# Kernel optimization log

Hardware: AMD Instinct MI355X
Metric: run time of the kernel (lower is better)

## Reference

```python
import jax, jax.numpy as jnp
import numpy as np

N_HEADS = 12

def setup_inputs() -> dict:
    key = jax.random.key(0)
    k1, k2, k3 = jax.random.split(key, 3)
    B, N, D = 2, 2048, 768
    x = jax.random.normal(k1, (B, N, D), dtype=jnp.float32)
    # Linear weights stored as [in, out] (equivalent to torch W.T)
    Wkqv = jax.random.normal(k2, (D, 3 * D), dtype=jnp.float32) * (1.0 / np.sqrt(D))
    bkqv = jnp.zeros((3 * D,), dtype=jnp.float32)
    Wproj = jax.random.normal(k3, (D, D), dtype=jnp.float32) * (1.0 / np.sqrt(D))
    bproj = jnp.zeros((D,), dtype=jnp.float32)
    return {"x": x, "Wkqv": Wkqv, "bkqv": bkqv, "Wproj": Wproj, "bproj": bproj}


def reference(x, Wkqv, bkqv, Wproj, bproj):
    B, N, D = x.shape
    H = N_HEADS
    hd = D // H
    kqv = x @ Wkqv + bkqv                     # [B, N, 3D]
    # NOTE: original chunks in (k, q, v) order
    k, q, v = jnp.split(kqv, 3, axis=-1)
    k = k.reshape(B, N, H, hd).transpose(0, 2, 1, 3)   # [B, H, N, hd]
    q = q.reshape(B, N, H, hd).transpose(0, 2, 1, 3)
    v = v.reshape(B, N, H, hd).transpose(0, 2, 1, 3)
    att = jnp.einsum('bhqd,bhkd->bhqk', q, k) / jnp.sqrt(jnp.float32(hd))
    causal = jnp.tril(jnp.ones((N, N), dtype=bool))    # [N, N]
    att = jnp.where(causal[None, None, :, :], att, jnp.float32(-jnp.inf))
    w = jax.nn.softmax(att, axis=-1)
    sa = jnp.einsum('bhqk,bhkd->bhqd', w, v)           # [B, H, N, hd]
    sa = sa.transpose(0, 2, 1, 3).reshape(B, N, D)
    return sa @ Wproj + bproj
```

## Files before the change

kernel.cpp:

```cpp
#include <hip/hip_runtime.h>

typedef __attribute__((ext_vector_type(8))) short bf16x8;
typedef __attribute__((ext_vector_type(16))) float f32x16;

#define BATCH 2
#define SEQ 2048
#define DMODEL 768
#define NH 12
#define HD 64
#define M_TOK (BATCH * SEQ)
#define N_KQV (3 * DMODEL)

#define GLOAD16(gsrc, ldst) __builtin_amdgcn_global_load_lds( \
    (const __attribute__((address_space(1))) unsigned int*)(const void*)(gsrc), \
    (__attribute__((address_space(3))) unsigned int*)(void*)(ldst), 16, 0, 0)

__device__ __forceinline__ unsigned short f2bf(float f) {
  unsigned int u = __float_as_uint(f);
  u += 0x7FFFu + ((u >> 16) & 1u);
  return (unsigned short)(u >> 16);
}

__device__ __forceinline__ unsigned int cvtpk(float lo, float hi) {
  unsigned int r;
  asm("v_cvt_pk_bf16_f32 %0, %1, %2" : "=v"(r) : "v"(lo), "v"(hi));
  return r;
}

#define NB_CVT 3072
#define NB_T1 (72 * 24)
#define NB_T2 (24 * 24)

__global__ __launch_bounds__(256) void prep_kernel(
    const float* __restrict__ x, unsigned short* __restrict__ x_bf,
    const float* __restrict__ Wkqv, unsigned short* __restrict__ wkqvT,
    const float* __restrict__ Wproj, unsigned short* __restrict__ wprojT) {
  const int b = blockIdx.x;
  if (b < NB_CVT) {
    int i = b * 256 + threadIdx.x;
    float4 v = reinterpret_cast<const float4*>(x)[i];
    unsigned long long p = (unsigned long long)f2bf(v.x)
                         | ((unsigned long long)f2bf(v.y) << 16)
                         | ((unsigned long long)f2bf(v.z) << 32)
                         | ((unsigned long long)f2bf(v.w) << 48);
    reinterpret_cast<unsigned long long*>(x_bf)[i] = p;
    return;
  }
  __shared__ float tile[32][33];
  const float* in;
  unsigned short* out;
  int rows, cols, bx, by;
  if (b < NB_CVT + NB_T1) {
    int j = b - NB_CVT;
    in = Wkqv; out = wkqvT; rows = DMODEL; cols = N_KQV;
    bx = j % 72; by = j / 72;
  } else {
    int j = b - NB_CVT - NB_T1;
    in = Wproj; out = wprojT; rows = DMODEL; cols = DMODEL;
    bx = j % 24; by = j / 24;
  }
  const int tx = threadIdx.x & 31, ty = threadIdx.x >> 5;
  int c0 = bx * 32, r0 = by * 32;
  for (int i = ty; i < 32; i += 8)
    tile[i][tx] = in[(size_t)(r0 + i) * cols + c0 + tx];
  __syncthreads();
  for (int i = ty; i < 32; i += 8)
    out[(size_t)(c0 + i) * rows + r0 + tx] = f2bf(tile[tx][i]);
}

template <int NBX, int MODE>
__global__ __launch_bounds__(64) void gemm_wi(
    const unsigned short* __restrict__ A,
    const unsigned short* __restrict__ BT,
    const float* __restrict__ bias,
    int NTOT,
    unsigned short* __restrict__ outK, unsigned short* __restrict__ outQ,
    unsigned short* __restrict__ outVT, float* __restrict__ outF) {
  constexpr int K = DMODEL;
  __shared__ __align__(16) unsigned short lds_a[2][64][32];
  __shared__ __align__(16) unsigned short lds_b[2][64][32];
  const int lane = threadIdx.x & 63;
  const int l31 = lane & 31, hi = lane >> 5;

  const int fid = (int)blockIdx.x;
  const int xcd = fid & 7, slot = fid >> 3;
  const int by = xcd * 8 + (slot & 7);
  const int bx = slot >> 3;
  const int m0 = by * 64, n0 = bx * 64;

  f32x16 acc[2][2];
#pragma unroll
  for (int mi = 0; mi < 2; mi++)
#pragma unroll
    for (int nj = 0; nj < 2; nj++)
#pragma unroll
      for (int i = 0; i < 16; i++) acc[mi][nj][i] = 0.f;

  const int srow = lane >> 2;
  const int sg = ((lane & 3) ^ ((lane >> 3) & 3)) * 8;
  const int xq = (l31 >> 1) & 3;

#define STAGE(buf, k0)                                                        \
  {                                                                           \
    _Pragma("unroll")                                                         \
    for (int rr = 0; rr < 4; ++rr)                                            \
      GLOAD16(&A[(size_t)(m0 + rr * 16 + srow) * K + (k0) + sg],              \
              &lds_a[buf][rr * 16][0]);                                       \
    _Pragma("unroll")                                                         \
    for (int rr = 0; rr < 4; ++rr)                                            \
      GLOAD16(&BT[(size_t)(n0 + rr * 16 + srow) * K + (k0) + sg],             \
              &lds_b[buf][rr * 16][0]);                                       \
  }

  const int KT = K >> 5;
  STAGE(0, 0);
  STAGE(1, 32);

  for (int kt = 0; kt < KT; ++kt) {
    const int cur = kt & 1;
    if (kt + 1 < KT) asm volatile("s_waitcnt vmcnt(8)" ::: "memory");
    else             asm volatile("s_waitcnt vmcnt(0)" ::: "memory");
    __builtin_amdgcn_sched_barrier(0);

    bf16x8 aA[2][2], aB[2][2];
#pragma unroll
    for (int ds = 0; ds < 2; ds++) {
      const int rc = ((ds * 2 + hi) ^ xq) * 8;
#pragma unroll
      for (int mi = 0; mi < 2; mi++)
        aA[ds][mi] = *(const bf16x8*)&lds_a[cur][mi * 32 + l31][rc];
#pragma unroll
      for (int nj = 0; nj < 2; nj++)
        aB[ds][nj] = *(const bf16x8*)&lds_b[cur][nj * 32 + l31][rc];
    }
#pragma unroll
    for (int ds = 0; ds < 2; ds++)
#pragma unroll
      for (int mi = 0; mi < 2; mi++)
#pragma unroll
        for (int nj = 0; nj < 2; nj++)
          acc[mi][nj] = __builtin_amdgcn_mfma_f32_32x32x16_bf16(
              aA[ds][mi], aB[ds][nj], acc[mi][nj], 0, 0, 0);

    if (kt + 2 < KT) {
      asm volatile("s_waitcnt lgkmcnt(0)" ::: "memory");
      __builtin_amdgcn_sched_barrier(0);
      STAGE(cur, (kt + 2) << 5);
    }
  }
#undef STAGE

#pragma unroll
  for (int mi = 0; mi < 2; mi++) {
#pragma unroll
    for (int nj = 0; nj < 2; nj++) {
#pragma unroll
      for (int r = 0; r < 16; r++) {
        int row = m0 + mi * 32 + (r & 3) + 8 * (r >> 2) + 4 * hi;
        int col = n0 + nj * 32 + l31;
        float v = acc[mi][nj][r] + bias[col];
        if (MODE == 0) {
          int chunk = col / DMODEL;
          int d = col - chunk * DMODEL;
          int hh = d >> 6, di = d & 63;
          int bb = row >> 11, tok = row & 2047;
          int bh = bb * NH + hh;
          if (chunk == 0)
            outK[((size_t)bh * SEQ + tok) * HD + di] = f2bf(v);
          else if (chunk == 1)
            outQ[((size_t)bh * SEQ + tok) * HD + di] = f2bf(v * 0.125f);
          else
            outVT[((size_t)bh * HD + di) * SEQ + tok] = f2bf(v);
        } else {
          outF[(size_t)row * NTOT + col] = v;
        }
      }
    }
  }
}

__global__ __launch_bounds__(128) void attn_kernel(
    const unsigned short* __restrict__ qbuf,
    const unsigned short* __restrict__ kbuf,
    const unsigned short* __restrict__ vT,
    unsigned short* __restrict__ sa) {
  __shared__ __align__(16) char smem_raw[18432];
  auto k_lds = reinterpret_cast<unsigned short (*)[72]>(smem_raw);
  auto v_lds = reinterpret_cast<unsigned short (*)[72]>(smem_raw + 9216);
  auto o_merge = reinterpret_cast<float (*)[32][33]>(smem_raw);
  auto l_merge = reinterpret_cast<float (*)[32]>(smem_raw + 9216);

  const int tid = threadIdx.x, lane = tid & 63, w = tid >> 6;
  const int l31 = lane & 31, hi = lane >> 5;

  const int fid = (int)blockIdx.y * (int)gridDim.x + (int)blockIdx.x;
  const int xcd = fid & 7, slot = fid >> 3;
  const int head3 = slot % 3;
  const int t = 63 - slot / 3;
  const int bh = head3 * 8 + xcd;
  const int ktmax = t >> 1;

  const size_t qk_base = (size_t)bh * SEQ * HD;
  const size_t v_base = (size_t)bh * HD * SEQ;
  const int bb = bh / NH, h = bh - bb * NH;

  const int sr = w * 32 + (lane >> 3);
  const int sc = (lane & 7) * 8;

  {
    bf16x8 rk[4], rv[4];
#pragma unroll
    for (int p = 0; p < 4; p++) {
      rk[p] = *(const bf16x8*)&kbuf[qk_base + (size_t)(sr + 8 * p) * HD + sc];
      rv[p] = *(const bf16x8*)&vT[v_base + (size_t)(sr + 8 * p) * SEQ + sc];
    }
#pragma unroll
    for (int p = 0; p < 4; p++) {
      *(bf16x8*)&k_lds[sr + 8 * p][sc] = rk[p];
      *(bf16x8*)&v_lds[sr + 8 * p][sc] = rv[p];
    }
  }

  bf16x8 aq[4];
#pragma unroll
  for (int ds = 0; ds < 4; ds++)
    aq[ds] = *(const bf16x8*)&qbuf[qk_base + (size_t)(t * 32 + l31) * HD + ds * 16 + hi * 8];

  f32x16 o0, o1;
#pragma unroll
  for (int i = 0; i < 16; i++) { o0[i] = 0.f; o1[i] = 0.f; }
  float lsum = 0.f;

  __syncthreads();

  for (int kt = 0; kt <= ktmax; ++kt) {
    const bool more = (kt < ktmax);
    bf16x8 rk[4], rv[4];
    if (more) {
      const int nrow = (kt + 1) * 64;
#pragma unroll
      for (int p = 0; p < 4; p++) {
        rk[p] = *(const bf16x8*)&kbuf[qk_base + (size_t)(nrow + sr + 8 * p) * HD + sc];
        rv[p] = *(const bf16x8*)&vT[v_base + (size_t)(sr + 8 * p) * SEQ + nrow + sc];
      }
    }

    f32x16 s;
#pragma unroll
    for (int i = 0; i < 16; i++) s[i] = 0.f;
    __builtin_amdgcn_s_setprio(1);
#pragma unroll
    for (int ds = 0; ds < 4; ds++) {
      bf16x8 bk = *(const bf16x8*)&k_lds[w * 32 + l31][ds * 16 + hi * 8];
      s = __builtin_amdgcn_mfma_f32_32x32x16_bf16(bk, aq[ds], s, 0, 0, 0);
    }
    __builtin_amdgcn_s_setprio(0);

    const bool diag = (kt == ktmax);
    const int qb2 = (t & 1) * 32;
#pragma unroll
    for (int r = 0; r < 16; r++) {
      int kr = (r & 3) + 8 * (r >> 2) + 4 * hi;
      float val = s[r];
      if (diag && (w * 32 + kr > qb2 + l31)) val = -1e30f;
      float p = __expf(val);
      s[r] = p;
      lsum += p;
    }

    union { unsigned int u[4]; bf16x8 v; } f1, f2;
    {
      unsigned int A = cvtpk(s[0], s[1]), B = cvtpk(s[2], s[3]);
      unsigned int C = cvtpk(s[4], s[5]), D = cvtpk(s[6], s[7]);
      auto rAC = __builtin_amdgcn_permlane32_swap(A, C, false, false);
      auto rBD = __builtin_amdgcn_permlane32_swap(B, D, false, false);
      f1.u[0] = rAC[0]; f1.u[1] = rBD[0]; f1.u[2] = rAC[1]; f1.u[3] = rBD[1];
      unsigned int A2 = cvtpk(s[8], s[9]),   B2 = cvtpk(s[10], s[11]);
      unsigned int C2 = cvtpk(s[12], s[13]), D2 = cvtpk(s[14], s[15]);
      auto rAC2 = __builtin_amdgcn_permlane32_swap(A2, C2, false, false);
      auto rBD2 = __builtin_amdgcn_permlane32_swap(B2, D2, false, false);
      f2.u[0] = rAC2[0]; f2.u[1] = rBD2[0]; f2.u[2] = rAC2[1]; f2.u[3] = rBD2[1];
    }

    __builtin_amdgcn_s_setprio(1);
    {
      bf16x8 bv00 = *(const bf16x8*)&v_lds[l31][w * 32 + hi * 8];
      bf16x8 bv01 = *(const bf16x8*)&v_lds[32 + l31][w * 32 + hi * 8];
      o0 = __builtin_amdgcn_mfma_f32_32x32x16_bf16(f1.v, bv00, o0, 0, 0, 0);
      o1 = __builtin_amdgcn_mfma_f32_32x32x16_bf16(f1.v, bv01, o1, 0, 0, 0);
      bf16x8 bv10 = *(const bf16x8*)&v_lds[l31][w * 32 + 16 + hi * 8];
      bf16x8 bv11 = *(const bf16x8*)&v_lds[32 + l31][w * 32 + 16 + hi * 8];
      o0 = __builtin_amdgcn_mfma_f32_32x32x16_bf16(f2.v, bv10, o0, 0, 0, 0);
      o1 = __builtin_amdgcn_mfma_f32_32x32x16_bf16(f2.v, bv11, o1, 0, 0, 0);
    }
    __builtin_amdgcn_s_setprio(0);

    if (more) {
      __syncthreads();
#pragma unroll
      for (int p = 0; p < 4; p++) {
        *(bf16x8*)&k_lds[sr + 8 * p][sc] = rk[p];
        *(bf16x8*)&v_lds[sr + 8 * p][sc] = rv[p];
      }
      __syncthreads();
    }
  }

  __syncthreads();
  {
    float ltot = lsum + __shfl_xor(lsum, 32);
    if (hi == 0) l_merge[w][l31] = ltot;
    f32x16 osend = w ? o0 : o1;
#pragma unroll
    for (int r = 0; r < 16; r++) {
      int ql = (r & 3) + 8 * (r >> 2) + 4 * hi;
      o_merge[w][ql][l31] = osend[r];
    }
    __syncthreads();
    f32x16 okeep = w ? o1 : o0;
#pragma unroll
    for (int r = 0; r < 16; r++) {
      int ql = (r & 3) + 8 * (r >> 2) + 4 * hi;
      float ot = okeep[r] + o_merge[1 - w][ql][l31];
      float lt = l_merge[0][ql] + l_merge[1][ql];
      sa[((size_t)bb * SEQ + t * 32 + ql) * DMODEL + h * HD + w * 32 + l31] = f2bf(ot / lt);
    }
  }
}


extern "C" void kernel_launch(void* const* d_in, const int* in_sizes, int n_in,
                              void* d_out, int out_size, void* d_ws, size_t ws_size,
                              hipStream_t stream) {
  const float* x     = (const float*)d_in[0];
  const float* Wkqv  = (const float*)d_in[1];
  const float* bkqv  = (const float*)d_in[2];
  const float* Wproj = (const float*)d_in[3];
  const float* bproj = (const float*)d_in[4];
  float* out = (float*)d_out;

  char* ws = (char*)d_ws;
  unsigned short* x_bf   = (unsigned short*)(ws + 0);
  unsigned short* wkqvT  = (unsigned short*)(ws + 6291456);
  unsigned short* wprojT = (unsigned short*)(ws + 9830400);
  unsigned short* qb     = (unsigned short*)(ws + 11010048);
  unsigned short* kb     = (unsigned short*)(ws + 17301504);
  unsigned short* vT     = (unsigned short*)(ws + 23592960);
  unsigned short* sa     = (unsigned short*)(ws + 29884416);

  prep_kernel<<<NB_CVT + NB_T1 + NB_T2, 256, 0, stream>>>(
      x, x_bf, Wkqv, wkqvT, Wproj, wprojT);

  gemm_wi<N_KQV / 64, 0><<<2304, 64, 0, stream>>>(
      x_bf, wkqvT, bkqv, N_KQV, kb, qb, vT, nullptr);

  attn_kernel<<<dim3(64, BATCH * NH), 128, 0, stream>>>(qb, kb, vT, sa);

  gemm_wi<DMODEL / 64, 1><<<768, 64, 0, stream>>>(
      sa, wprojT, bproj, DMODEL, nullptr, nullptr, nullptr, out);
}
```

Before: 99.73 us.

## Split attention over key chunks with atomic accumulation and a finalize pass

The attention kernel now splits each query tile's causal key range into chunks of up to 8 key tiles, giving 3840 blocks instead of 1536, which balances the triangular workload. Partial unnormalised outputs and row sums are combined with float atomicAdd into zeroed fp32 buffers, and the zeroing is folded into the prep kernel. A new finalize kernel divides by the row sums and writes bf16 output. This depends on the softmax skipping max subtraction, so partials can be added directly. It costs an extra kernel launch, about 12.5 MB of zeroing and atomic traffic, and makes the summation order nondeterministic.

```diff
diff --git a/kernel.cpp b/kernel.cpp
--- a/kernel.cpp
+++ b/kernel.cpp
@@ -10,6 +10,7 @@
 #define HD 64
 #define M_TOK (BATCH * SEQ)
 #define N_KQV (3 * DMODEL)
+#define BH_TOT (BATCH * NH)
 
 #define GLOAD16(gsrc, ldst) __builtin_amdgcn_global_load_lds( \
     (const __attribute__((address_space(1))) unsigned int*)(const void*)(gsrc), \
@@ -30,11 +31,14 @@
 #define NB_CVT 3072
 #define NB_T1 (72 * 24)
 #define NB_T2 (24 * 24)
+#define NFLOAT_ACC (BH_TOT * SEQ * HD + BH_TOT * SEQ)
+#define NB_Z (NFLOAT_ACC / 4 / 256)
 
 __global__ __launch_bounds__(256) void prep_kernel(
     const float* __restrict__ x, unsigned short* __restrict__ x_bf,
     const float* __restrict__ Wkqv, unsigned short* __restrict__ wkqvT,
-    const float* __restrict__ Wproj, unsigned short* __restrict__ wprojT) {
+    const float* __restrict__ Wproj, unsigned short* __restrict__ wprojT,
+    float* __restrict__ acc_zero) {
   const int b = blockIdx.x;
   if (b < NB_CVT) {
     int i = b * 256 + threadIdx.x;
@@ -44,6 +48,11 @@
                          | ((unsigned long long)f2bf(v.z) << 32)
                          | ((unsigned long long)f2bf(v.w) << 48);
     reinterpret_cast<unsigned long long*>(x_bf)[i] = p;
+    return;
+  }
+  if (b >= NB_CVT + NB_T1 + NB_T2) {
+    int i = (b - NB_CVT - NB_T1 - NB_T2) * 256 + threadIdx.x;
+    reinterpret_cast<float4*>(acc_zero)[i] = (float4){0.f, 0.f, 0.f, 0.f};
     return;
   }
   __shared__ float tile[32][33];
@@ -183,7 +192,8 @@
     const unsigned short* __restrict__ qbuf,
     const unsigned short* __restrict__ kbuf,
     const unsigned short* __restrict__ vT,
-    unsigned short* __restrict__ sa) {
+    float* __restrict__ O_acc,
+    float* __restrict__ l_acc) {
   __shared__ __align__(16) char smem_raw[18432];
   auto k_lds = reinterpret_cast<unsigned short (*)[72]>(smem_raw);
   auto v_lds = reinterpret_cast<unsigned short (*)[72]>(smem_raw + 9216);
@@ -193,16 +203,23 @@
   const int tid = threadIdx.x, lane = tid & 63, w = tid >> 6;
   const int l31 = lane & 31, hi = lane >> 5;
 
-  const int fid = (int)blockIdx.y * (int)gridDim.x + (int)blockIdx.x;
+  const int fid = (int)blockIdx.x;
   const int xcd = fid & 7, slot = fid >> 3;
   const int head3 = slot % 3;
-  const int t = 63 - slot / 3;
+  const int s = slot / 3;
+  int c, r_;
+  if (s < 64)       { c = 0; r_ = s; }
+  else if (s < 112) { c = 1; r_ = s - 64; }
+  else if (s < 144) { c = 2; r_ = s - 112; }
+  else              { c = 3; r_ = s - 144; }
+  const int t = 63 - r_;
   const int bh = head3 * 8 + xcd;
   const int ktmax = t >> 1;
+  const int kt0 = c * 8;
+  const int kt_end = (kt0 + 7 < ktmax) ? kt0 + 7 : ktmax;
 
   const size_t qk_base = (size_t)bh * SEQ * HD;
   const size_t v_base = (size_t)bh * HD * SEQ;
-  const int bb = bh / NH, h = bh - bb * NH;
 
   const int sr = w * 32 + (lane >> 3);
   const int sc = (lane & 7) * 8;
@@ -211,8 +228,8 @@
     bf16x8 rk[4], rv[4];
 #pragma unroll
     for (int p = 0; p < 4; p++) {
-      rk[p] = *(const bf16x8*)&kbuf[qk_base + (size_t)(sr + 8 * p) * HD + sc];
-      rv[p] = *(const bf16x8*)&vT[v_base + (size_t)(sr + 8 * p) * SEQ + sc];
+      rk[p] = *(const bf16x8*)&kbuf[qk_base + (size_t)(kt0 * 64 + sr + 8 * p) * HD + sc];
+      rv[p] = *(const bf16x8*)&vT[v_base + (size_t)(sr + 8 * p) * SEQ + kt0 * 64 + sc];
     }
 #pragma unroll
     for (int p = 0; p < 4; p++) {
@@ -233,8 +250,8 @@
 
   __syncthreads();
 
-  for (int kt = 0; kt <= ktmax; ++kt) {
-    const bool more = (kt < ktmax);
+  for (int kt = kt0; kt <= kt_end; ++kt) {
+    const bool more = (kt < kt_end);
     bf16x8 rk[4], rv[4];
     if (more) {
       const int nrow = (kt + 1) * 64;
@@ -245,14 +262,14 @@
       }
     }
 
-    f32x16 s;
-#pragma unroll
-    for (int i = 0; i < 16; i++) s[i] = 0.f;
+    f32x16 sv;
+#pragma unroll
+    for (int i = 0; i < 16; i++) sv[i] = 0.f;
     __builtin_amdgcn_s_setprio(1);
 #pragma unroll
     for (int ds = 0; ds < 4; ds++) {
       bf16x8 bk = *(const bf16x8*)&k_lds[w * 32 + l31][ds * 16 + hi * 8];
-      s = __builtin_amdgcn_mfma_f32_32x32x16_bf16(bk, aq[ds], s, 0, 0, 0);
+      sv = __builtin_amdgcn_mfma_f32_32x32x16_bf16(bk, aq[ds], sv, 0, 0, 0);
     }
     __builtin_amdgcn_s_setprio(0);
 
@@ -261,22 +278,22 @@
 #pragma unroll
     for (int r = 0; r < 16; r++) {
       int kr = (r & 3) + 8 * (r >> 2) + 4 * hi;
-      float val = s[r];
+      float val = sv[r];
       if (diag && (w * 32 + kr > qb2 + l31)) val = -1e30f;
       float p = __expf(val);
-      s[r] = p;
+      sv[r] = p;
       lsum += p;
     }
 
     union { unsigned int u[4]; bf16x8 v; } f1, f2;
     {
-      unsigned int A = cvtpk(s[0], s[1]), B = cvtpk(s[2], s[3]);
-      unsigned int C = cvtpk(s[4], s[5]), D = cvtpk(s[6], s[7]);
+      unsigned int A = cvtpk(sv[0], sv[1]), B = cvtpk(sv[2], sv[3]);
+      unsigned int C = cvtpk(sv[4], sv[5]), D = cvtpk(sv[6], sv[7]);
       auto rAC = __builtin_amdgcn_permlane32_swap(A, C, false, false);
       auto rBD = __builtin_amdgcn_permlane32_swap(B, D, false, false);
       f1.u[0] = rAC[0]; f1.u[1] = rBD[0]; f1.u[2] = rAC[1]; f1.u[3] = rBD[1];
-      unsigned int A2 = cvtpk(s[8], s[9]),   B2 = cvtpk(s[10], s[11]);
-      unsigned int C2 = cvtpk(s[12], s[13]), D2 = cvtpk(s[14], s[15]);
+      unsigned int A2 = cvtpk(sv[8], sv[9]),   B2 = cvtpk(sv[10], sv[11]);
+      unsigned int C2 = cvtpk(sv[12], sv[13]), D2 = cvtpk(sv[14], sv[15]);
       auto rAC2 = __builtin_amdgcn_permlane32_swap(A2, C2, false, false);
       auto rBD2 = __builtin_amdgcn_permlane32_swap(B2, D2, false, false);
       f2.u[0] = rAC2[0]; f2.u[1] = rBD2[0]; f2.u[2] = rAC2[1]; f2.u[3] = rBD2[1];
@@ -322,10 +339,25 @@
     for (int r = 0; r < 16; r++) {
       int ql = (r & 3) + 8 * (r >> 2) + 4 * hi;
       float ot = okeep[r] + o_merge[1 - w][ql][l31];
-      float lt = l_merge[0][ql] + l_merge[1][ql];
-      sa[((size_t)bb * SEQ + t * 32 + ql) * DMODEL + h * HD + w * 32 + l31] = f2bf(ot / lt);
-    }
-  }
+      atomicAdd(&O_acc[((size_t)bh * SEQ + t * 32 + ql) * HD + w * 32 + l31], ot);
+      if (w == 0 && l31 == 0) {
+        float lt = l_merge[0][ql] + l_merge[1][ql];
+        atomicAdd(&l_acc[(size_t)bh * SEQ + t * 32 + ql], lt);
+      }
+    }
+  }
+}
+
+__global__ __launch_bounds__(256) void attn_finalize(
+    const float* __restrict__ O_acc, const float* __restrict__ l_acc,
+    unsigned short* __restrict__ sa) {
+  int e = blockIdx.x * 256 + threadIdx.x;
+  int d = e & 63;
+  int row = (e >> 6) & 2047;
+  int bh = e >> 17;
+  int bb = bh / NH, h = bh - bb * NH;
+  float v = O_acc[e] / l_acc[bh * SEQ + row];
+  sa[((size_t)bb * SEQ + row) * DMODEL + h * HD + d] = f2bf(v);
 }
 
 
@@ -347,14 +379,18 @@
   unsigned short* kb     = (unsigned short*)(ws + 17301504);
   unsigned short* vT     = (unsigned short*)(ws + 23592960);
   unsigned short* sa     = (unsigned short*)(ws + 29884416);
-
-  prep_kernel<<<NB_CVT + NB_T1 + NB_T2, 256, 0, stream>>>(
-      x, x_bf, Wkqv, wkqvT, Wproj, wprojT);
+  float* O_acc           = (float*)(ws + 36175872);
+  float* l_acc           = (float*)(ws + 48758784);
+
+  prep_kernel<<<NB_CVT + NB_T1 + NB_T2 + NB_Z, 256, 0, stream>>>(
+      x, x_bf, Wkqv, wkqvT, Wproj, wprojT, O_acc);
 
   gemm_wi<N_KQV / 64, 0><<<2304, 64, 0, stream>>>(
       x_bf, wkqvT, bkqv, N_KQV, kb, qb, vT, nullptr);
 
-  attn_kernel<<<dim3(64, BATCH * NH), 128, 0, stream>>>(qb, kb, vT, sa);
+  attn_kernel<<<3840, 128, 0, stream>>>(qb, kb, vT, O_acc, l_acc);
+
+  attn_finalize<<<BH_TOT * SEQ * HD / 256, 256, 0, stream>>>(O_acc, l_acc, sa);
 
   gemm_wi<DMODEL / 64, 1><<<768, 64, 0, stream>>>(
       sa, wprojT, bproj, DMODEL, nullptr, nullptr, nullptr, out);
```

Measured after the change: 126.4 us. 26.7% more time.
